# Kernel tuning notes

Measured on AMD Instinct MI355X. Metric: run time of the kernel, lower is better.

## Reference

```python
import jax, jax.numpy as jnp
import numpy as np

LN_EPS = 1e-5
TOP_K = 2


def setup_inputs() -> dict:
    key = jax.random.key(0)
    ks = jax.random.split(key, 6)
    B, S, D, I, E = 4, 1024, 1024, 4096, 8
    return {
        "hidden_states": jax.random.normal(ks[0], (B, S, D), dtype=jnp.float32),
        "attention_mask": jnp.ones((B, S), dtype=jnp.float32),
        "gate_w": jax.random.normal(ks[1], (E, D), dtype=jnp.float32) * 0.02,
        "w1": jax.random.normal(ks[2], (E, D, I), dtype=jnp.float32) * 0.02,
        "b1": jnp.zeros((E, I), dtype=jnp.float32),
        "w2": jax.random.normal(ks[3], (E, I, D), dtype=jnp.float32) * 0.02,
        "b2": jnp.zeros((E, D), dtype=jnp.float32),
        "ln_gamma": jnp.ones((D,), dtype=jnp.float32),
        "ln_beta": jnp.zeros((D,), dtype=jnp.float32),
    }


def reference(hidden_states, attention_mask, gate_w, w1, b1, w2, b2, ln_gamma, ln_beta):
    B, S, D = hidden_states.shape
    E = gate_w.shape[0]
    h = hidden_states.reshape(-1, D).astype(jnp.float32)  # (T, D)

    # --- gate: softmax over experts, top-2, renormalize ---
    logits = h @ gate_w.T                                  # (T, E)
    probs = jax.nn.softmax(logits, axis=-1)
    rw, sel = jax.lax.top_k(probs, TOP_K)                  # (T, k), (T, k)
    rw = rw / jnp.sum(rw, axis=-1, keepdims=True)

    # per-token dense combine weights: (T, E), zero for non-selected experts
    onehot = jax.nn.one_hot(sel, E, dtype=rw.dtype)        # (T, k, E)
    w_te = jnp.einsum('tk,tke->te', rw, onehot)            # (T, E)

    # --- expert FFNs (dense over all experts; weights zero-out non-selected) ---
    mid = jax.nn.gelu(jnp.einsum('td,edi->eti', h, w1) + b1[:, None, :], approximate=False)
    eout = jnp.einsum('eti,eid->etd', mid, w2) + b2[:, None, :]  # (E, T, D)
    moe_out = jnp.einsum('etd,te->td', eout, w_te)         # (T, D)

    out = moe_out.reshape(B, S, D) * attention_mask[..., None]
    out = hidden_states + out

    # LayerNorm
    mu = jnp.mean(out, axis=-1, keepdims=True)
    var = jnp.var(out, axis=-1, keepdims=True)
    out = (out - mu) * jax.lax.rsqrt(var + LN_EPS) * ln_gamma + ln_beta

    # load balancing loss: mse(expert_usage, uniform)
    T = h.shape[0]
    usage = jnp.sum(onehot, axis=(0, 1)) / T               # (E,)
    aux_loss = jnp.mean((usage - 1.0 / E) ** 2)
    return out, aux_loss
```

## Files before the change

### kernel.cpp

```cpp
#include <hip/hip_runtime.h>
#include <hip/hip_bf16.h>
#include <math.h>

#define T_TOK 4096
#define D_DIM 1024
#define I_DIM 4096
#define E_EXP 8
#define MAX_TILES 72

typedef __attribute__((ext_vector_type(8))) short bf16x8;
typedef __attribute__((ext_vector_type(4))) float f32x4;

__device__ __forceinline__ unsigned short f2bf(float x) {
    unsigned int u = __float_as_uint(x);
    u += 0x7fffu + ((u >> 16) & 1u);
    return (unsigned short)(u >> 16);
}

__device__ __forceinline__ void glds16(const unsigned short* g, unsigned short* l) {
    __builtin_amdgcn_global_load_lds(
        (const __attribute__((address_space(1))) unsigned int*)g,
        (__attribute__((address_space(3))) unsigned int*)(unsigned int)(unsigned long long)(void*)l,
        16, 0, 0);
}

__global__ void gate_kernel(const float* __restrict__ h, const float* __restrict__ gw,
                            int* __restrict__ counts, int* __restrict__ sel,
                            float* __restrict__ wgt) {
    int t = blockIdx.x;
    int tid = threadIdx.x;
    float acc[E_EXP];
#pragma unroll
    for (int e = 0; e < E_EXP; e++) acc[e] = 0.f;
    const float* hr = h + (size_t)t * D_DIM;
    for (int d = tid; d < D_DIM; d += 256) {
        float hv = hr[d];
#pragma unroll
        for (int e = 0; e < E_EXP; e++) acc[e] += hv * gw[e * D_DIM + d];
    }
#pragma unroll
    for (int e = 0; e < E_EXP; e++)
        for (int off = 32; off > 0; off >>= 1) acc[e] += __shfl_down(acc[e], off, 64);
    __shared__ float red[4][E_EXP];
    int wave = tid >> 6, lane = tid & 63;
    if (lane == 0) {
#pragma unroll
        for (int e = 0; e < E_EXP; e++) red[wave][e] = acc[e];
    }
    __syncthreads();
    if (tid == 0) {
        float lg[E_EXP];
#pragma unroll
        for (int e = 0; e < E_EXP; e++) lg[e] = red[0][e] + red[1][e] + red[2][e] + red[3][e];
        float mx = lg[0];
#pragma unroll
        for (int e = 1; e < E_EXP; e++) mx = fmaxf(mx, lg[e]);
        float p[E_EXP];
#pragma unroll
        for (int e = 0; e < E_EXP; e++) p[e] = expf(lg[e] - mx);
        int i0 = 0; float b0 = p[0];
#pragma unroll
        for (int e = 1; e < E_EXP; e++) if (p[e] > b0) { b0 = p[e]; i0 = e; }
        int i1 = -1; float b1v = -1.f;
#pragma unroll
        for (int e = 0; e < E_EXP; e++) if (e != i0 && p[e] > b1v) { b1v = p[e]; i1 = e; }
        float den = b0 + b1v;
        sel[2 * t] = i0; sel[2 * t + 1] = i1;
        wgt[2 * t] = b0 / den; wgt[2 * t + 1] = b1v / den;
        atomicAdd(&counts[i0], 1);
        atomicAdd(&counts[i1], 1);
    }
}

__global__ void offsets_kernel(const int* __restrict__ counts, int* __restrict__ offs,
                               int* __restrict__ cursors, float* __restrict__ aux_out,
                               int* __restrict__ tile_e, int* __restrict__ tile_m,
                               int* __restrict__ ntiles) {
    if (blockIdx.x == 0 && threadIdx.x == 0) {
        int off = 0; float aux = 0.f; int nt = 0;
        for (int e = 0; e < E_EXP; e++) {
            offs[e] = off; off += counts[e]; cursors[e] = 0;
            float u = (float)counts[e] / (float)T_TOK;
            float d = u - 1.0f / (float)E_EXP;
            aux += d * d;
            for (int m0 = 0; m0 < counts[e]; m0 += 128) {
                tile_e[nt] = e; tile_m[nt] = m0; nt++;
            }
        }
        ntiles[0] = nt;
        aux_out[0] = aux / (float)E_EXP;
    }
}

__global__ void scatter_kernel(const int* __restrict__ sel, const float* __restrict__ wgt,
                               const int* __restrict__ offs, int* __restrict__ cursors,
                               int* __restrict__ tok_list, float* __restrict__ tok_w,
                               int* __restrict__ slot_of) {
    int t = blockIdx.x * 256 + threadIdx.x;
    if (t >= T_TOK) return;
#pragma unroll
    for (int k = 0; k < 2; k++) {
        int e = sel[2 * t + k];
        int pos = atomicAdd(&cursors[e], 1);
        int idx = offs[e] + pos;
        tok_list[idx] = t;
        tok_w[idx] = wgt[2 * t + k];
        slot_of[2 * t + k] = idx;
    }
}

__global__ void cvtH_kernel(const float* __restrict__ src, unsigned short* __restrict__ dst) {
    size_t i = ((size_t)blockIdx.x * 256 + threadIdx.x) * 8;
    float4 a = *(const float4*)(src + i);
    float4 b = *(const float4*)(src + i + 4);
    union { unsigned short u[8]; uint4 v; } o;
    o.u[0] = f2bf(a.x); o.u[1] = f2bf(a.y); o.u[2] = f2bf(a.z); o.u[3] = f2bf(a.w);
    o.u[4] = f2bf(b.x); o.u[5] = f2bf(b.y); o.u[6] = f2bf(b.z); o.u[7] = f2bf(b.w);
    *(uint4*)(dst + i) = o.v;
}

__global__ void transpose_cvt_kernel(const float* __restrict__ src, unsigned short* __restrict__ dst,
                                     int R, int C) {
    __shared__ float tile[32][33];
    int e = blockIdx.z;
    const float* s = src + (size_t)e * R * C;
    unsigned short* d = dst + (size_t)e * R * C;
    int c0 = blockIdx.x * 32, r0 = blockIdx.y * 32;
    int tx = threadIdx.x, ty = threadIdx.y;
#pragma unroll
    for (int j = 0; j < 4; j++)
        tile[ty + 8 * j][tx] = s[(size_t)(r0 + ty + 8 * j) * C + c0 + tx];
    __syncthreads();
#pragma unroll
    for (int j = 0; j < 4; j++)
        d[(size_t)(c0 + ty + 8 * j) * R + r0 + tx] = f2bf(tile[tx][ty + 8 * j]);
}

template <int MODE>
__launch_bounds__(256)
__global__ void moe_gemm_kernel(const unsigned short* __restrict__ Abase,
                                const unsigned short* __restrict__ Bt,
                                const float* __restrict__ bias,
                                const int* __restrict__ counts, const int* __restrict__ offs,
                                const int* __restrict__ tile_e, const int* __restrict__ tile_m,
                                const int* __restrict__ ntiles,
                                const int* __restrict__ tok_list, const float* __restrict__ tok_w,
                                unsigned short* __restrict__ midout, float* __restrict__ slotbuf) {
    constexpr int K = (MODE == 0) ? D_DIM : I_DIM;
    constexpr int N = (MODE == 0) ? I_DIM : D_DIM;
    const int tix = blockIdx.x;
    if (tix >= ntiles[0]) return;
    const int e = tile_e[tix];
    const int m0 = tile_m[tix];
    const int Ne = counts[e];
    const int n0 = blockIdx.y * 128;
    const int seg = offs[e];

    __shared__ __align__(16) unsigned short lA[128 * 32];
    __shared__ __align__(16) unsigned short lB[128 * 32];

    const int tid = threadIdx.x;
    const int lane = tid & 63;
    const int wave = tid >> 6;
    const int wm = (wave >> 1) * 64;
    const int wn = (wave & 1) * 64;
    const int quad = lane >> 4;
    const int l15 = lane & 15;

    const int srow = wave * 32 + (lane >> 2);
    const int scol = (lane & 3) * 8;

    const unsigned short *pA0, *pA1;
    {
        int mr0 = m0 + srow, mr1 = mr0 + 16;
        size_t arow0, arow1;
        if (MODE == 0) {
            arow0 = (size_t)tok_list[seg + (mr0 < Ne ? mr0 : 0)] * K;
            arow1 = (size_t)tok_list[seg + (mr1 < Ne ? mr1 : 0)] * K;
        } else {
            arow0 = (size_t)(seg + (mr0 < Ne ? mr0 : 0)) * K;
            arow1 = (size_t)(seg + (mr1 < Ne ? mr1 : 0)) * K;
        }
        pA0 = Abase + arow0 + scol;
        pA1 = Abase + arow1 + scol;
    }
    const unsigned short* Bte = Bt + (size_t)e * N * K;
    const unsigned short* pB0 = Bte + (size_t)(n0 + srow) * K + scol;
    const unsigned short* pB1 = Bte + (size_t)(n0 + srow + 16) * K + scol;

    unsigned short* dA0 = lA + (wave * 32) * 32;
    unsigned short* dA1 = lA + (wave * 32 + 16) * 32;
    unsigned short* dB0 = lB + (wave * 32) * 32;
    unsigned short* dB1 = lB + (wave * 32 + 16) * 32;

    f32x4 acc[4][4];
#pragma unroll
    for (int i = 0; i < 4; i++)
#pragma unroll
        for (int j = 0; j < 4; j++) acc[i][j] = (f32x4){0.f, 0.f, 0.f, 0.f};

    for (int k0 = 0; k0 < K; k0 += 32) {
        glds16(pA0, dA0);
        glds16(pA1, dA1);
        glds16(pB0, dB0);
        glds16(pB1, dB1);
        pA0 += 32; pA1 += 32; pB0 += 32; pB1 += 32;
        __syncthreads();
        bf16x8 af[4], bfr[4];
#pragma unroll
        for (int i = 0; i < 4; i++)
            af[i] = *(const bf16x8*)&lA[(wm + i * 16 + l15) * 32 + quad * 8];
#pragma unroll
        for (int j = 0; j < 4; j++)
            bfr[j] = *(const bf16x8*)&lB[(wn + j * 16 + l15) * 32 + quad * 8];
#pragma unroll
        for (int i = 0; i < 4; i++)
#pragma unroll
            for (int j = 0; j < 4; j++)
                acc[i][j] = __builtin_amdgcn_mfma_f32_16x16x32_bf16(af[i], bfr[j], acc[i][j], 0, 0, 0);
        __syncthreads();
    }

    const float* be = bias + (size_t)e * N;
#pragma unroll
    for (int i = 0; i < 4; i++) {
        int mbase = m0 + wm + i * 16 + quad * 4;
#pragma unroll
        for (int j = 0; j < 4; j++) {
            int n = n0 + wn + j * 16 + l15;
            float bv = be[n];
#pragma unroll
            for (int r = 0; r < 4; r++) {
                int m = mbase + r;
                if (m < Ne) {
                    float v = acc[i][j][r] + bv;
                    if (MODE == 0) {
                        v = 0.5f * v * (1.0f + erff(v * 0.70710678118654752f));
                        midout[(size_t)(seg + m) * N + n] = f2bf(v);
                    } else {
                        slotbuf[(size_t)(seg + m) * N + n] = tok_w[seg + m] * v;
                    }
                }
            }
        }
    }
}

__global__ void ln_kernel(const float* __restrict__ hs, const float* __restrict__ mask,
                          const float* __restrict__ slotbuf, const int* __restrict__ slot_of,
                          const float* __restrict__ gamma, const float* __restrict__ beta,
                          float* __restrict__ outp) {
    int t = blockIdx.x, tid = threadIdx.x;
    int s0 = slot_of[2 * t], s1 = slot_of[2 * t + 1];
    float mk = mask[t];
    const float4* hr = (const float4*)(hs + (size_t)t * D_DIM);
    const float4* p0 = (const float4*)(slotbuf + (size_t)s0 * D_DIM);
    const float4* p1 = (const float4*)(slotbuf + (size_t)s1 * D_DIM);
    float4 hv = hr[tid], a = p0[tid], b = p1[tid];
    float x0 = hv.x + mk * (a.x + b.x);
    float x1 = hv.y + mk * (a.y + b.y);
    float x2 = hv.z + mk * (a.z + b.z);
    float x3 = hv.w + mk * (a.w + b.w);
    float sum = x0 + x1 + x2 + x3;
    float sq = x0 * x0 + x1 * x1 + x2 * x2 + x3 * x3;
    for (int off = 32; off > 0; off >>= 1) {
        sum += __shfl_down(sum, off, 64);
        sq += __shfl_down(sq, off, 64);
    }
    __shared__ float rsum[4], rsq[4];
    __shared__ float mu_s, rstd_s;
    int wave = tid >> 6, lane = tid & 63;
    if (lane == 0) { rsum[wave] = sum; rsq[wave] = sq; }
    __syncthreads();
    if (tid == 0) {
        float s = rsum[0] + rsum[1] + rsum[2] + rsum[3];
        float q = rsq[0] + rsq[1] + rsq[2] + rsq[3];
        float mu = s / (float)D_DIM;
        float var = q / (float)D_DIM - mu * mu;
        mu_s = mu; rstd_s = rsqrtf(var + 1e-5f);
    }
    __syncthreads();
    float mu = mu_s, rstd = rstd_s;
    const float4* g4 = (const float4*)gamma;
    const float4* b4 = (const float4*)beta;
    float4 g = g4[tid], bb = b4[tid];
    float4 o;
    o.x = (x0 - mu) * rstd * g.x + bb.x;
    o.y = (x1 - mu) * rstd * g.y + bb.y;
    o.z = (x2 - mu) * rstd * g.z + bb.z;
    o.w = (x3 - mu) * rstd * g.w + bb.w;
    ((float4*)(outp + (size_t)t * D_DIM))[tid] = o;
}

extern "C" void kernel_launch(void* const* d_in, const int* in_sizes, int n_in,
                              void* d_out, int out_size, void* d_ws, size_t ws_size,
                              hipStream_t stream) {
    const float* hs    = (const float*)d_in[0];
    const float* mask  = (const float*)d_in[1];
    const float* gw    = (const float*)d_in[2];
    const float* w1    = (const float*)d_in[3];
    const float* b1    = (const float*)d_in[4];
    const float* w2    = (const float*)d_in[5];
    const float* b2    = (const float*)d_in[6];
    const float* gamma = (const float*)d_in[7];
    const float* beta  = (const float*)d_in[8];
    float* out = (float*)d_out;

    char* ws = (char*)d_ws;
    int*   counts   = (int*)(ws + 0);
    int*   cursors  = (int*)(ws + 64);
    int*   offs     = (int*)(ws + 128);
    int*   ntiles   = (int*)(ws + 256);
    int*   tile_e   = (int*)(ws + 512);
    int*   tile_m   = (int*)(ws + 1024);
    int*   sel      = (int*)(ws + 4096);
    float* wgt      = (float*)(ws + 4096 + 1 * 32768);
    int*   slot_of  = (int*)(ws + 4096 + 2 * 32768);
    int*   tok_list = (int*)(ws + 4096 + 3 * 32768);
    float* tok_w    = (float*)(ws + 4096 + 4 * 32768);
    unsigned short* Hbf = (unsigned short*)(ws + (1ull << 20));
    unsigned short* W1t = (unsigned short*)(ws + (9ull << 20));
    unsigned short* W2t = (unsigned short*)(ws + (73ull << 20));
    unsigned short* mid = (unsigned short*)(ws + (137ull << 20));
    float* slotbuf      = (float*)(ws + (201ull << 20));

    hipMemsetAsync(counts, 0, 64, stream);
    gate_kernel<<<T_TOK, 256, 0, stream>>>(hs, gw, counts, sel, wgt);
    offsets_kernel<<<1, 64, 0, stream>>>(counts, offs, cursors, out + (size_t)T_TOK * D_DIM,
                                         tile_e, tile_m, ntiles);
    scatter_kernel<<<T_TOK / 256, 256, 0, stream>>>(sel, wgt, offs, cursors, tok_list, tok_w, slot_of);
    cvtH_kernel<<<(T_TOK * D_DIM / 8) / 256, 256, 0, stream>>>(hs, Hbf);
    transpose_cvt_kernel<<<dim3(I_DIM / 32, D_DIM / 32, E_EXP), dim3(32, 8), 0, stream>>>(w1, W1t, D_DIM, I_DIM);
    transpose_cvt_kernel<<<dim3(D_DIM / 32, I_DIM / 32, E_EXP), dim3(32, 8), 0, stream>>>(w2, W2t, I_DIM, D_DIM);
    moe_gemm_kernel<0><<<dim3(MAX_TILES, I_DIM / 128), 256, 0, stream>>>(
        Hbf, W1t, b1, counts, offs, tile_e, tile_m, ntiles, tok_list, tok_w, mid, nullptr);
    moe_gemm_kernel<1><<<dim3(MAX_TILES, D_DIM / 128), 256, 0, stream>>>(
        mid, W2t, b2, counts, offs, tile_e, tile_m, ntiles, tok_list, tok_w, nullptr, slotbuf);
    ln_kernel<<<T_TOK, 256, 0, stream>>>(hs, mask, slotbuf, slot_of, gamma, beta, out);
}
```

Baseline: 764.3 us.

## Split MoE GEMM kernels, vectorize transposes, stage GELU output through LDS

Replaces the 32x32 weight transpose with a 64x64 tile version that uses float4 loads and 16-byte bf16 stores. Splits the templated GEMM into two kernels. The first uses a polynomial erf approximation in GELU and writes the bf16 intermediate through shared memory as coalesced 16-byte stores. The second uses a narrower 64-column N tile to launch more blocks for the down projection. These changes target the transpose bandwidth, the scattered epilogue stores and low occupancy in the second GEMM, at the cost of a small erf approximation error and extra LDS syncs.

```diff
diff --git a/kernel.cpp b/kernel.cpp
--- a/kernel.cpp
+++ b/kernel.cpp
@@ -15,6 +15,15 @@
     unsigned int u = __float_as_uint(x);
     u += 0x7fffu + ((u >> 16) & 1u);
     return (unsigned short)(u >> 16);
+}
+
+__device__ __forceinline__ float fast_erf(float x) {
+    float ax = fabsf(x);
+    float t = __fdividef(1.0f, fmaf(0.3275911f, ax, 1.0f));
+    float y = t * fmaf(t, fmaf(t, fmaf(t, fmaf(t, 1.061405429f, -1.453152027f),
+                                       1.421413741f), -0.284496736f), 0.254829592f);
+    float r = 1.0f - y * __expf(-ax * ax);
+    return copysignf(r, x);
 }
 
 __device__ __forceinline__ void glds16(const unsigned short* g, unsigned short* l) {
@@ -119,35 +128,45 @@
     *(uint4*)(dst + i) = o.v;
 }
 
-__global__ void transpose_cvt_kernel(const float* __restrict__ src, unsigned short* __restrict__ dst,
-                                     int R, int C) {
-    __shared__ float tile[32][33];
+__global__ void transpose_cvt64(const float* __restrict__ src, unsigned short* __restrict__ dst,
+                                int R, int C) {
+    __shared__ float tile[64][65];
     int e = blockIdx.z;
     const float* s = src + (size_t)e * R * C;
     unsigned short* d = dst + (size_t)e * R * C;
-    int c0 = blockIdx.x * 32, r0 = blockIdx.y * 32;
-    int tx = threadIdx.x, ty = threadIdx.y;
-#pragma unroll
-    for (int j = 0; j < 4; j++)
-        tile[ty + 8 * j][tx] = s[(size_t)(r0 + ty + 8 * j) * C + c0 + tx];
+    int c0 = blockIdx.x * 64, r0 = blockIdx.y * 64;
+    int tid = threadIdx.x;
+    int lr = tid >> 4;
+    int lc = (tid & 15) * 4;
+#pragma unroll
+    for (int rr = 0; rr < 64; rr += 16) {
+        float4 v = *(const float4*)&s[(size_t)(r0 + lr + rr) * C + c0 + lc];
+        tile[lr + rr][lc] = v.x; tile[lr + rr][lc + 1] = v.y;
+        tile[lr + rr][lc + 2] = v.z; tile[lr + rr][lc + 3] = v.w;
+    }
     __syncthreads();
 #pragma unroll
-    for (int j = 0; j < 4; j++)
-        d[(size_t)(c0 + ty + 8 * j) * R + r0 + tx] = f2bf(tile[tx][ty + 8 * j]);
-}
-
-template <int MODE>
+    for (int q = tid; q < 512; q += 256) {
+        int c = q >> 3;
+        int rch = (q & 7) * 8;
+        union { unsigned short u[8]; uint4 v; } o;
+#pragma unroll
+        for (int j = 0; j < 8; j++) o.u[j] = f2bf(tile[rch + j][c]);
+        *(uint4*)&d[(size_t)(c0 + c) * R + r0 + rch] = o.v;
+    }
+}
+
 __launch_bounds__(256)
-__global__ void moe_gemm_kernel(const unsigned short* __restrict__ Abase,
-                                const unsigned short* __restrict__ Bt,
-                                const float* __restrict__ bias,
-                                const int* __restrict__ counts, const int* __restrict__ offs,
-                                const int* __restrict__ tile_e, const int* __restrict__ tile_m,
-                                const int* __restrict__ ntiles,
-                                const int* __restrict__ tok_list, const float* __restrict__ tok_w,
-                                unsigned short* __restrict__ midout, float* __restrict__ slotbuf) {
-    constexpr int K = (MODE == 0) ? D_DIM : I_DIM;
-    constexpr int N = (MODE == 0) ? I_DIM : D_DIM;
+__global__ void moe_gemm1_kernel(const unsigned short* __restrict__ Abase,
+                                 const unsigned short* __restrict__ Bt,
+                                 const float* __restrict__ bias,
+                                 const int* __restrict__ counts, const int* __restrict__ offs,
+                                 const int* __restrict__ tile_e, const int* __restrict__ tile_m,
+                                 const int* __restrict__ ntiles,
+                                 const int* __restrict__ tok_list,
+                                 unsigned short* __restrict__ midout) {
+    constexpr int K = D_DIM;
+    constexpr int N = I_DIM;
     const int tix = blockIdx.x;
     if (tix >= ntiles[0]) return;
     const int e = tile_e[tix];
@@ -156,8 +175,9 @@
     const int n0 = blockIdx.y * 128;
     const int seg = offs[e];
 
-    __shared__ __align__(16) unsigned short lA[128 * 32];
-    __shared__ __align__(16) unsigned short lB[128 * 32];
+    __shared__ __align__(16) unsigned short smem[8192];
+    unsigned short* lA = smem;
+    unsigned short* lB = smem + 4096;
 
     const int tid = threadIdx.x;
     const int lane = tid & 63;
@@ -173,14 +193,8 @@
     const unsigned short *pA0, *pA1;
     {
         int mr0 = m0 + srow, mr1 = mr0 + 16;
-        size_t arow0, arow1;
-        if (MODE == 0) {
-            arow0 = (size_t)tok_list[seg + (mr0 < Ne ? mr0 : 0)] * K;
-            arow1 = (size_t)tok_list[seg + (mr1 < Ne ? mr1 : 0)] * K;
-        } else {
-            arow0 = (size_t)(seg + (mr0 < Ne ? mr0 : 0)) * K;
-            arow1 = (size_t)(seg + (mr1 < Ne ? mr1 : 0)) * K;
-        }
+        size_t arow0 = (size_t)tok_list[seg + (mr0 < Ne ? mr0 : 0)] * K;
+        size_t arow1 = (size_t)tok_list[seg + (mr1 < Ne ? mr1 : 0)] * K;
         pA0 = Abase + arow0 + scol;
         pA1 = Abase + arow1 + scol;
     }
@@ -223,10 +237,117 @@
 
     const float* be = bias + (size_t)e * N;
 #pragma unroll
+    for (int p = 0; p < 2; p++) {
+        if ((wave & 1) == p) {
+#pragma unroll
+            for (int i = 0; i < 4; i++) {
+                int mloc = wm + i * 16 + quad * 4;
+#pragma unroll
+                for (int j = 0; j < 4; j++) {
+                    int nh = j * 16 + l15;
+                    float bv = be[n0 + p * 64 + nh];
+#pragma unroll
+                    for (int r = 0; r < 4; r++) {
+                        float v = acc[i][j][r] + bv;
+                        v = 0.5f * v * (1.0f + fast_erf(v * 0.70710678118654752f));
+                        smem[(mloc + r) * 64 + nh] = f2bf(v);
+                    }
+                }
+            }
+        }
+        __syncthreads();
+#pragma unroll
+        for (int q = tid; q < 1024; q += 256) {
+            int row = q >> 3, sg = q & 7;
+            if (m0 + row < Ne) {
+                uint4 v = *(const uint4*)&smem[row * 64 + sg * 8];
+                *(uint4*)&midout[(size_t)(seg + m0 + row) * N + n0 + p * 64 + sg * 8] = v;
+            }
+        }
+        __syncthreads();
+    }
+}
+
+__launch_bounds__(256)
+__global__ void moe_gemm2_kernel(const unsigned short* __restrict__ Abase,
+                                 const unsigned short* __restrict__ Bt,
+                                 const float* __restrict__ bias,
+                                 const int* __restrict__ counts, const int* __restrict__ offs,
+                                 const int* __restrict__ tile_e, const int* __restrict__ tile_m,
+                                 const int* __restrict__ ntiles,
+                                 const float* __restrict__ tok_w,
+                                 float* __restrict__ slotbuf) {
+    constexpr int K = I_DIM;
+    constexpr int N = D_DIM;
+    const int tix = blockIdx.x;
+    if (tix >= ntiles[0]) return;
+    const int e = tile_e[tix];
+    const int m0 = tile_m[tix];
+    const int Ne = counts[e];
+    const int n0 = blockIdx.y * 64;
+    const int seg = offs[e];
+
+    __shared__ __align__(16) unsigned short lA[128 * 32];
+    __shared__ __align__(16) unsigned short lB[64 * 32];
+
+    const int tid = threadIdx.x;
+    const int lane = tid & 63;
+    const int wave = tid >> 6;
+    const int wm = (wave >> 1) * 64;
+    const int wn = (wave & 1) * 32;
+    const int quad = lane >> 4;
+    const int l15 = lane & 15;
+
+    const int srowA = wave * 32 + (lane >> 2);
+    const int srowB = wave * 16 + (lane >> 2);
+    const int scol = (lane & 3) * 8;
+
+    const unsigned short *pA0, *pA1;
+    {
+        int mr0 = m0 + srowA, mr1 = mr0 + 16;
+        pA0 = Abase + (size_t)(seg + (mr0 < Ne ? mr0 : 0)) * K + scol;
+        pA1 = Abase + (size_t)(seg + (mr1 < Ne ? mr1 : 0)) * K + scol;
+    }
+    const unsigned short* Bte = Bt + (size_t)e * N * K;
+    const unsigned short* pB0 = Bte + (size_t)(n0 + srowB) * K + scol;
+
+    unsigned short* dA0 = lA + (wave * 32) * 32;
+    unsigned short* dA1 = lA + (wave * 32 + 16) * 32;
+    unsigned short* dB0 = lB + (wave * 16) * 32;
+
+    f32x4 acc[4][2];
+#pragma unroll
+    for (int i = 0; i < 4; i++)
+#pragma unroll
+        for (int j = 0; j < 2; j++) acc[i][j] = (f32x4){0.f, 0.f, 0.f, 0.f};
+
+    for (int k0 = 0; k0 < K; k0 += 32) {
+        glds16(pA0, dA0);
+        glds16(pA1, dA1);
+        glds16(pB0, dB0);
+        pA0 += 32; pA1 += 32; pB0 += 32;
+        __syncthreads();
+        bf16x8 af[4], bfr[2];
+#pragma unroll
+        for (int i = 0; i < 4; i++)
+            af[i] = *(const bf16x8*)&lA[(wm + i * 16 + l15) * 32 + quad * 8];
+#pragma unroll
+        for (int j = 0; j < 2; j++)
+            bfr[j] = *(const bf16x8*)&lB[(wn + j * 16 + l15) * 32 + quad * 8];
+#pragma unroll
+        for (int i = 0; i < 4; i++)
+#pragma unroll
+            for (int j = 0; j < 2; j++)
+                acc[i][j] = __builtin_amdgcn_mfma_f32_16x16x32_bf16(af[i], bfr[j], acc[i][j], 0, 0, 0);
+        __syncthreads();
+    }
+
+    const float* be = bias + (size_t)e * N;
+#pragma unroll
     for (int i = 0; i < 4; i++) {
         int mbase = m0 + wm + i * 16 + quad * 4;
 #pragma unroll
-        for (int j = 0; j < 4; j++) {
+        for (int j = 0; j < 2; j++) {
             int n = n0 + wn + j * 16 + l15;
             float bv = be[n];
 #pragma unroll
@@ -234,12 +355,7 @@
                 int m = mbase + r;
                 if (m < Ne) {
                     float v = acc[i][j][r] + bv;
-                    if (MODE == 0) {
-                        v = 0.5f * v * (1.0f + erff(v * 0.70710678118654752f));
-                        midout[(size_t)(seg + m) * N + n] = f2bf(v);
-                    } else {
-                        slotbuf[(size_t)(seg + m) * N + n] = tok_w[seg + m] * v;
-                    }
+                    slotbuf[(size_t)(seg + m) * N + n] = tok_w[seg + m] * v;
                 }
             }
         }
@@ -330,11 +446,11 @@
                                          tile_e, tile_m, ntiles);
     scatter_kernel<<<T_TOK / 256, 256, 0, stream>>>(sel, wgt, offs, cursors, tok_list, tok_w, slot_of);
     cvtH_kernel<<<(T_TOK * D_DIM / 8) / 256, 256, 0, stream>>>(hs, Hbf);
-    transpose_cvt_kernel<<<dim3(I_DIM / 32, D_DIM / 32, E_EXP), dim3(32, 8), 0, stream>>>(w1, W1t, D_DIM, I_DIM);
-    transpose_cvt_kernel<<<dim3(D_DIM / 32, I_DIM / 32, E_EXP), dim3(32, 8), 0, stream>>>(w2, W2t, I_DIM, D_DIM);
-    moe_gemm_kernel<0><<<dim3(MAX_TILES, I_DIM / 128), 256, 0, stream>>>(
-        Hbf, W1t, b1, counts, offs, tile_e, tile_m, ntiles, tok_list, tok_w, mid, nullptr);
-    moe_gemm_kernel<1><<<dim3(MAX_TILES, D_DIM / 128), 256, 0, stream>>>(
-        mid, W2t, b2, counts, offs, tile_e, tile_m, ntiles, tok_list, tok_w, nullptr, slotbuf);
+    transpose_cvt64<<<dim3(I_DIM / 64, D_DIM / 64, E_EXP), 256, 0, stream>>>(w1, W1t, D_DIM, I_DIM);
+    transpose_cvt64<<<dim3(D_DIM / 64, I_DIM / 64, E_EXP), 256, 0, stream>>>(w2, W2t, I_DIM, D_DIM);
+    moe_gemm1_kernel<<<dim3(MAX_TILES, I_DIM / 128), 256, 0, stream>>>(
+        Hbf, W1t, b1, counts, offs, tile_e, tile_m, ntiles, tok_list, mid);
+    moe_gemm2_kernel<<<dim3(MAX_TILES, D_DIM / 64), 256, 0, stream>>>(
+        mid, W2t, b2, counts, offs, tile_e, tile_m, ntiles, tok_w, slotbuf);
     ln_kernel<<<T_TOK, 256, 0, stream>>>(hs, mask, slotbuf, slot_of, gamma, beta, out);
 }
```

After: 837.2 us. +9.5%, slower.

## Shrink GEMM N-tile, fuse bf16 cast into gate, widen transpose, fast erf

Applied to the files above, without the earlier changes.

Several changes are bundled. The expert GEMMs now use a 128x64 tile instead of 128x128, with an occupancy hint of 5 blocks per SM, which gives more blocks and better occupancy at the cost of less operand reuse. The hidden-state bf16 conversion moves into the gate kernel, removing a separate pass, and the gate dot products are vectorized. The weight transpose-convert kernels use 64x64 tiles with float4 loads and 16-byte stores. Exact erff in the GELU is replaced by the Abramowitz-Stegun polynomial approximation, which adds small numerical error.

```diff
diff --git a/kernel.cpp b/kernel.cpp
--- a/kernel.cpp
+++ b/kernel.cpp
@@ -17,6 +17,15 @@
     return (unsigned short)(u >> 16);
 }
 
+__device__ __forceinline__ float fast_erf(float x) {
+    float ax = fabsf(x);
+    float t = __fdividef(1.0f, fmaf(0.3275911f, ax, 1.0f));
+    float y = t * fmaf(t, fmaf(t, fmaf(t, fmaf(t, 1.061405429f, -1.453152027f),
+                                       1.421413741f), -0.284496736f), 0.254829592f);
+    float r = 1.0f - y * __expf(-ax * ax);
+    return copysignf(r, x);
+}
+
 __device__ __forceinline__ void glds16(const unsigned short* g, unsigned short* l) {
     __builtin_amdgcn_global_load_lds(
         (const __attribute__((address_space(1))) unsigned int*)g,
@@ -26,17 +35,22 @@
 
 __global__ void gate_kernel(const float* __restrict__ h, const float* __restrict__ gw,
                             int* __restrict__ counts, int* __restrict__ sel,
-                            float* __restrict__ wgt) {
+                            float* __restrict__ wgt, unsigned short* __restrict__ Hbf) {
     int t = blockIdx.x;
     int tid = threadIdx.x;
+    const float* hr = h + (size_t)t * D_DIM;
+    float4 hv4 = *(const float4*)&hr[tid * 4];
+
+    union { unsigned short u[4]; uint2 v; } ob;
+    ob.u[0] = f2bf(hv4.x); ob.u[1] = f2bf(hv4.y);
+    ob.u[2] = f2bf(hv4.z); ob.u[3] = f2bf(hv4.w);
+    *(uint2*)&Hbf[(size_t)t * D_DIM + tid * 4] = ob.v;
+
     float acc[E_EXP];
 #pragma unroll
-    for (int e = 0; e < E_EXP; e++) acc[e] = 0.f;
-    const float* hr = h + (size_t)t * D_DIM;
-    for (int d = tid; d < D_DIM; d += 256) {
-        float hv = hr[d];
-#pragma unroll
-        for (int e = 0; e < E_EXP; e++) acc[e] += hv * gw[e * D_DIM + d];
+    for (int e = 0; e < E_EXP; e++) {
+        float4 g4 = *(const float4*)&gw[e * D_DIM + tid * 4];
+        acc[e] = hv4.x * g4.x + hv4.y * g4.y + hv4.z * g4.z + hv4.w * g4.w;
     }
 #pragma unroll
     for (int e = 0; e < E_EXP; e++)
@@ -109,35 +123,36 @@
     }
 }
 
-__global__ void cvtH_kernel(const float* __restrict__ src, unsigned short* __restrict__ dst) {
-    size_t i = ((size_t)blockIdx.x * 256 + threadIdx.x) * 8;
-    float4 a = *(const float4*)(src + i);
-    float4 b = *(const float4*)(src + i + 4);
-    union { unsigned short u[8]; uint4 v; } o;
-    o.u[0] = f2bf(a.x); o.u[1] = f2bf(a.y); o.u[2] = f2bf(a.z); o.u[3] = f2bf(a.w);
-    o.u[4] = f2bf(b.x); o.u[5] = f2bf(b.y); o.u[6] = f2bf(b.z); o.u[7] = f2bf(b.w);
-    *(uint4*)(dst + i) = o.v;
-}
-
-__global__ void transpose_cvt_kernel(const float* __restrict__ src, unsigned short* __restrict__ dst,
-                                     int R, int C) {
-    __shared__ float tile[32][33];
+__global__ void transpose_cvt64(const float* __restrict__ src, unsigned short* __restrict__ dst,
+                                int R, int C) {
+    __shared__ float tile[64][65];
     int e = blockIdx.z;
     const float* s = src + (size_t)e * R * C;
     unsigned short* d = dst + (size_t)e * R * C;
-    int c0 = blockIdx.x * 32, r0 = blockIdx.y * 32;
-    int tx = threadIdx.x, ty = threadIdx.y;
-#pragma unroll
-    for (int j = 0; j < 4; j++)
-        tile[ty + 8 * j][tx] = s[(size_t)(r0 + ty + 8 * j) * C + c0 + tx];
+    int c0 = blockIdx.x * 64, r0 = blockIdx.y * 64;
+    int tid = threadIdx.x;
+    int lr = tid >> 4;
+    int lc = (tid & 15) * 4;
+#pragma unroll
+    for (int rr = 0; rr < 64; rr += 16) {
+        float4 v = *(const float4*)&s[(size_t)(r0 + lr + rr) * C + c0 + lc];
+        tile[lr + rr][lc] = v.x; tile[lr + rr][lc + 1] = v.y;
+        tile[lr + rr][lc + 2] = v.z; tile[lr + rr][lc + 3] = v.w;
+    }
     __syncthreads();
 #pragma unroll
-    for (int j = 0; j < 4; j++)
-        d[(size_t)(c0 + ty + 8 * j) * R + r0 + tx] = f2bf(tile[tx][ty + 8 * j]);
+    for (int q = tid; q < 512; q += 256) {
+        int c = q >> 3;
+        int rch = (q & 7) * 8;
+        union { unsigned short u[8]; uint4 v; } o;
+#pragma unroll
+        for (int j = 0; j < 8; j++) o.u[j] = f2bf(tile[rch + j][c]);
+        *(uint4*)&d[(size_t)(c0 + c) * R + r0 + rch] = o.v;
+    }
 }
 
 template <int MODE>
-__launch_bounds__(256)
+__launch_bounds__(256, 5)
 __global__ void moe_gemm_kernel(const unsigned short* __restrict__ Abase,
                                 const unsigned short* __restrict__ Bt,
                                 const float* __restrict__ bias,
@@ -153,26 +168,26 @@
     const int e = tile_e[tix];
     const int m0 = tile_m[tix];
     const int Ne = counts[e];
-    const int n0 = blockIdx.y * 128;
+    const int n0 = blockIdx.y * 64;
     const int seg = offs[e];
 
     __shared__ __align__(16) unsigned short lA[128 * 32];
-    __shared__ __align__(16) unsigned short lB[128 * 32];
+    __shared__ __align__(16) unsigned short lB[64 * 32];
 
     const int tid = threadIdx.x;
     const int lane = tid & 63;
     const int wave = tid >> 6;
     const int wm = (wave >> 1) * 64;
-    const int wn = (wave & 1) * 64;
+    const int wn = (wave & 1) * 32;
     const int quad = lane >> 4;
     const int l15 = lane & 15;
 
-    const int srow = wave * 32 + (lane >> 2);
+    const int lrow = lane >> 2;
     const int scol = (lane & 3) * 8;
 
-    const unsigned short *pA0, *pA1;
+    const unsigned short *pA0, *pA1, *pB0;
     {
-        int mr0 = m0 + srow, mr1 = mr0 + 16;
+        int mr0 = m0 + wave * 32 + lrow, mr1 = mr0 + 16;
         size_t arow0, arow1;
         if (MODE == 0) {
             arow0 = (size_t)tok_list[seg + (mr0 < Ne ? mr0 : 0)] * K;
@@ -185,38 +200,35 @@
         pA1 = Abase + arow1 + scol;
     }
     const unsigned short* Bte = Bt + (size_t)e * N * K;
-    const unsigned short* pB0 = Bte + (size_t)(n0 + srow) * K + scol;
-    const unsigned short* pB1 = Bte + (size_t)(n0 + srow + 16) * K + scol;
+    pB0 = Bte + (size_t)(n0 + wave * 16 + lrow) * K + scol;
 
     unsigned short* dA0 = lA + (wave * 32) * 32;
     unsigned short* dA1 = lA + (wave * 32 + 16) * 32;
-    unsigned short* dB0 = lB + (wave * 32) * 32;
-    unsigned short* dB1 = lB + (wave * 32 + 16) * 32;
-
-    f32x4 acc[4][4];
+    unsigned short* dB0 = lB + (wave * 16) * 32;
+
+    f32x4 acc[4][2];
 #pragma unroll
     for (int i = 0; i < 4; i++)
 #pragma unroll
-        for (int j = 0; j < 4; j++) acc[i][j] = (f32x4){0.f, 0.f, 0.f, 0.f};
+        for (int j = 0; j < 2; j++) acc[i][j] = (f32x4){0.f, 0.f, 0.f, 0.f};
 
     for (int k0 = 0; k0 < K; k0 += 32) {
         glds16(pA0, dA0);
         glds16(pA1, dA1);
         glds16(pB0, dB0);
-        glds16(pB1, dB1);
-        pA0 += 32; pA1 += 32; pB0 += 32; pB1 += 32;
+        pA0 += 32; pA1 += 32; pB0 += 32;
         __syncthreads();
-        bf16x8 af[4], bfr[4];
+        bf16x8 af[4], bfr[2];
 #pragma unroll
         for (int i = 0; i < 4; i++)
             af[i] = *(const bf16x8*)&lA[(wm + i * 16 + l15) * 32 + quad * 8];
 #pragma unroll
-        for (int j = 0; j < 4; j++)
+        for (int j = 0; j < 2; j++)
             bfr[j] = *(const bf16x8*)&lB[(wn + j * 16 + l15) * 32 + quad * 8];
 #pragma unroll
         for (int i = 0; i < 4; i++)
 #pragma unroll
-            for (int j = 0; j < 4; j++)
+            for (int j = 0; j < 2; j++)
                 acc[i][j] = __builtin_amdgcn_mfma_f32_16x16x32_bf16(af[i], bfr[j], acc[i][j], 0, 0, 0);
         __syncthreads();
     }
@@ -226,7 +238,7 @@
     for (int i = 0; i < 4; i++) {
         int mbase = m0 + wm + i * 16 + quad * 4;
 #pragma unroll
-        for (int j = 0; j < 4; j++) {
+        for (int j = 0; j < 2; j++) {
             int n = n0 + wn + j * 16 + l15;
             float bv = be[n];
 #pragma unroll
@@ -235,7 +247,7 @@
                 if (m < Ne) {
                     float v = acc[i][j][r] + bv;
                     if (MODE == 0) {
-                        v = 0.5f * v * (1.0f + erff(v * 0.70710678118654752f));
+                        v = 0.5f * v * (1.0f + fast_erf(v * 0.70710678118654752f));
                         midout[(size_t)(seg + m) * N + n] = f2bf(v);
                     } else {
                         slotbuf[(size_t)(seg + m) * N + n] = tok_w[seg + m] * v;
@@ -325,16 +337,15 @@
     float* slotbuf      = (float*)(ws + (201ull << 20));
 
     hipMemsetAsync(counts, 0, 64, stream);
-    gate_kernel<<<T_TOK, 256, 0, stream>>>(hs, gw, counts, sel, wgt);
+    gate_kernel<<<T_TOK, 256, 0, stream>>>(hs, gw, counts, sel, wgt, Hbf);
     offsets_kernel<<<1, 64, 0, stream>>>(counts, offs, cursors, out + (size_t)T_TOK * D_DIM,
                                          tile_e, tile_m, ntiles);
     scatter_kernel<<<T_TOK / 256, 256, 0, stream>>>(sel, wgt, offs, cursors, tok_list, tok_w, slot_of);
-    cvtH_kernel<<<(T_TOK * D_DIM / 8) / 256, 256, 0, stream>>>(hs, Hbf);
-    transpose_cvt_kernel<<<dim3(I_DIM / 32, D_DIM / 32, E_EXP), dim3(32, 8), 0, stream>>>(w1, W1t, D_DIM, I_DIM);
-    transpose_cvt_kernel<<<dim3(D_DIM / 32, I_DIM / 32, E_EXP), dim3(32, 8), 0, stream>>>(w2, W2t, I_DIM, D_DIM);
-    moe_gemm_kernel<0><<<dim3(MAX_TILES, I_DIM / 128), 256, 0, stream>>>(
+    transpose_cvt64<<<dim3(I_DIM / 64, D_DIM / 64, E_EXP), 256, 0, stream>>>(w1, W1t, D_DIM, I_DIM);
+    transpose_cvt64<<<dim3(D_DIM / 64, I_DIM / 64, E_EXP), 256, 0, stream>>>(w2, W2t, I_DIM, D_DIM);
+    moe_gemm_kernel<0><<<dim3(MAX_TILES, I_DIM / 64), 256, 0, stream>>>(
         Hbf, W1t, b1, counts, offs, tile_e, tile_m, ntiles, tok_list, tok_w, mid, nullptr);
-    moe_gemm_kernel<1><<<dim3(MAX_TILES, D_DIM / 128), 256, 0, stream>>>(
+    moe_gemm_kernel<1><<<dim3(MAX_TILES, D_DIM / 64), 256, 0, stream>>>(
         mid, W2t, b2, counts, offs, tile_e, tile_m, ntiles, tok_list, tok_w, nullptr, slotbuf);
     ln_kernel<<<T_TOK, 256, 0, stream>>>(hs, mask, slotbuf, slot_of, gamma, beta, out);
 }
```

After: 787.4 us. +3.0%, slower.
